# Performance work log

Measured on AMD Instinct MI355X. Metric: run time of the kernel, lower is better.

Reference implementation:

```python
import jax, jax.numpy as jnp
import numpy as np

B, S, D, H = 1, 4096, 1024, 16
HD = D // H  # head_size = 64

def setup_inputs() -> dict:
    key = jax.random.key(0)
    ks = jax.random.split(key, 9)
    scale = 1.0 / np.sqrt(D)
    return {
        "x": jax.random.normal(ks[0], (B, S, D), jnp.float32),
        "Wq": jax.random.normal(ks[1], (D, D), jnp.float32) * scale,
        "bq": jax.random.normal(ks[2], (D,), jnp.float32) * 0.01,
        "Wk": jax.random.normal(ks[3], (D, D), jnp.float32) * scale,
        "bk": jax.random.normal(ks[4], (D,), jnp.float32) * 0.01,
        "Wv": jax.random.normal(ks[5], (D, D), jnp.float32) * scale,
        "bv": jax.random.normal(ks[6], (D,), jnp.float32) * 0.01,
        "Wo": jax.random.normal(ks[7], (D, D), jnp.float32) * scale,
        "bo": jax.random.normal(ks[8], (D,), jnp.float32) * 0.01,
    }

def _split_heads(t):
    # (B, S, D) -> (B, H, S, HD)
    return t.reshape(B, S, H, HD).transpose(0, 2, 1, 3)

def reference(x, Wq, bq, Wk, bk, Wv, bv, Wo, bo):
    q = _split_heads(x @ Wq + bq)
    k = _split_heads(x @ Wk + bk)
    v = _split_heads(x @ Wv + bv)
    # scores: (B, H, S, S), materialized as in the original naive attention
    scores = jnp.einsum('bhqd,bhkd->bhqk', q, k) / jnp.sqrt(jnp.asarray(HD, q.dtype))
    causal = jnp.tril(jnp.ones((S, S), dtype=bool))  # tril mask, broadcast over (B, H)
    scores = jnp.where(causal[None, None], scores, jnp.asarray(-1e9, scores.dtype))
    attn = jax.nn.softmax(scores, axis=-1)
    out = jnp.einsum('bhqk,bhkd->bhqd', attn, v)  # (B, H, S, HD)
    out = out.transpose(0, 2, 1, 3).reshape(B, S, D)  # combine heads
    return out @ Wo + bo
```

## Files before the change

kernel.cpp:

```cpp
#include <hip/hip_runtime.h>

#define SEQ 4096
#define DM  1024
#define NH  16
#define HDIM 64

typedef unsigned short u16;
typedef unsigned int   u32;
typedef __bf16 bf16x8 __attribute__((ext_vector_type(8)));
typedef float f32x4 __attribute__((ext_vector_type(4)));

__device__ __forceinline__ float bf2f(u16 u) {
    unsigned v = ((unsigned)u) << 16;
    float f;
    __builtin_memcpy(&f, &v, 4);
    return f;
}
__device__ __forceinline__ u16 f2bf(float f) {
    unsigned u;
    __builtin_memcpy(&u, &f, 4);
    return (u16)((u + 0x7fffu + ((u >> 16) & 1u)) >> 16);
}
__device__ __forceinline__ u32 bfpack(float a, float b) {
    u32 ua, ub;
    __builtin_memcpy(&ua, &a, 4);
    __builtin_memcpy(&ub, &b, 4);
    return ((ua + 0x8000u) >> 16) | ((ub + 0x8000u) & 0xffff0000u);
}

typedef const __attribute__((address_space(1))) unsigned int gas_uint;
typedef __attribute__((address_space(3))) unsigned int las_uint;
__device__ __forceinline__ void gld16(const u16* g, u16* l) {
    __builtin_amdgcn_global_load_lds((gas_uint*)g, (las_uint*)l, 16, 0, 0);
}

__device__ __forceinline__ f32x4 mfma16(bf16x8 a, bf16x8 b, f32x4 c) {
    return __builtin_amdgcn_mfma_f32_16x16x32_bf16(a, b, c, 0, 0, 0);
}

#define QSCALE 0.18033688011f

__device__ __forceinline__ int self_detect(const void* in, int tid, int* sflag) {
    if (tid == 0) *sflag = 0;
    __syncthreads();
    const u16* p = (const u16*)in;
    int loc = 0;
    for (int i = tid; i < 4096; i += 256) {
        float v = fabsf(bf2f(p[i]));
        if (v < 3e38f && v > 1e4f) loc = 1;
    }
    if (loc) *sflag = 1;
    __syncthreads();
    return *sflag;
}

__global__ __launch_bounds__(256) void prep_all(const void* w0, const void* w1,
                                                const void* w2, const void* w3,
                                                const void* b0, const void* b1,
                                                const void* b2, const void* b3,
                                                const void* xin,
                                                u16* __restrict__ wt,
                                                u16* __restrict__ b_dst,
                                                u16* __restrict__ xc,
                                                int* __restrict__ flags) {
    __shared__ int sflag;
    __shared__ u16 tile[32][33];
    const int z   = blockIdx.z;
    const int tid = threadIdx.x;
    const void* srcs[5] = {w0, w1, w2, w3, xin};
    const void* in = srcs[z];
    const int f = self_detect(in, tid, &sflag);

    if (z == 4) {
        const int p = blockIdx.y * 32 + blockIdx.x;
        if (p == 0 && tid == 0) flags[0] = f;
#pragma unroll
        for (int c = 0; c < 2; ++c) {
            const size_t i = (size_t)p * 4096 + c * 2048 + tid * 8;
            if (f) {
                const float4* s4 = (const float4*)((const float*)in + i);
                float4 a = s4[0], bq = s4[1];
                uint4 o;
                o.x = bfpack(a.x, a.y);
                o.y = bfpack(a.z, a.w);
                o.z = bfpack(bq.x, bq.y);
                o.w = bfpack(bq.z, bq.w);
                *(uint4*)(xc + i) = o;
            } else {
                *(uint4*)(xc + i) = *(const uint4*)((const u16*)in + i);
            }
        }
        return;
    }

    const void* bins[4] = {b0, b1, b2, b3};
    u16* out = wt + (size_t)z * DM * DM;
    const float scale = (z == 0) ? QSCALE : 1.0f;
    const int bx = blockIdx.x * 32;
    const int by = blockIdx.y * 32;
    const int tx = tid & 31;
    const int ty = tid >> 5;
#pragma unroll
    for (int i = ty; i < 32; i += 8) {
        size_t idx = (size_t)(by + i) * DM + bx + tx;
        float v = f ? ((const float*)in)[idx] : bf2f(((const u16*)in)[idx]);
        tile[i][tx] = f2bf(v * scale);
    }
    __syncthreads();
#pragma unroll
    for (int i = ty; i < 32; i += 8) out[(size_t)(bx + i) * DM + by + tx] = tile[tx][i];

    if (blockIdx.x == 0 && blockIdx.y == 0) {
        const void* bi = bins[z];
        for (int i = tid; i < DM; i += 256) {
            float v = f ? ((const float*)bi)[i] : bf2f(((const u16*)bi)[i]);
            b_dst[z * DM + i] = f2bf(v * scale);
        }
    }
}

__global__ __launch_bounds__(256, 2) void gemm_qkv(const u16* __restrict__ A,
                                                   const u16* __restrict__ Bt,
                                                   const u16* __restrict__ bias,
                                                   u16* __restrict__ Qo,
                                                   u16* __restrict__ Ko,
                                                   u16* __restrict__ VtO) {
    __shared__ u16 As[128 * 32];
    __shared__ u16 Bs[128 * 32];
    const int tid  = threadIdx.x;
    const int lane = tid & 63;
    const int w    = tid >> 6;
    const int m    = lane & 15;
    const int quad = lane >> 4;
    const int wr   = w >> 1;
    const int wc   = w & 1;

    const int b   = blockIdx.x;
    const int x   = b & 7;
    const int j   = b >> 3;
    const int nb  = (x * 3 + j % 3) * 128;
    const int mb  = (j / 3) * 128;
    const int mat = nb >> 10;
    const int lnb = nb & 1023;

    f32x4 acc[4][4] = {};

    for (int kb = 0; kb < DM; kb += 32) {
        __syncthreads();
#pragma unroll
        for (int i = 0; i < 2; ++i) {
            const int Lb = i * 256 + w * 64;
            const int L  = Lb + lane;
            const int row = L >> 2, cb = L & 3;
            gld16(&A[(size_t)(mb + row) * DM + kb + cb * 8], &As[Lb * 8]);
            gld16(&Bt[(size_t)(nb + row) * DM + kb + cb * 8], &Bs[Lb * 8]);
        }
        __syncthreads();

        bf16x8 af[4];
#pragma unroll
        for (int mt = 0; mt < 4; ++mt)
            af[mt] = *(const bf16x8*)&As[(wr * 64 + mt * 16 + m) * 32 + quad * 8];
#pragma unroll
        for (int ct = 0; ct < 4; ++ct) {
            bf16x8 bfr = *(const bf16x8*)&Bs[(wc * 64 + ct * 16 + m) * 32 + quad * 8];
#pragma unroll
            for (int mt = 0; mt < 4; ++mt)
                acc[mt][ct] = mfma16(af[mt], bfr, acc[mt][ct]);
        }
    }

    if (mat < 2) {
        u16* C = mat ? Ko : Qo;
#pragma unroll
        for (int ct = 0; ct < 4; ++ct) {
            float bv = bf2f(bias[nb + wc * 64 + ct * 16 + m]);
#pragma unroll
            for (int mt = 0; mt < 4; ++mt)
#pragma unroll
                for (int r = 0; r < 4; ++r) {
                    int row = mb + wr * 64 + mt * 16 + quad * 4 + r;
                    C[(size_t)row * DM + lnb + wc * 64 + ct * 16 + m] =
                        f2bf(acc[mt][ct][r] + bv);
                }
        }
    } else {
#pragma unroll
        for (int ct = 0; ct < 4; ++ct) {
            const int n = lnb + wc * 64 + ct * 16 + m;
            float bv = bf2f(bias[nb + wc * 64 + ct * 16 + m]);
#pragma unroll
            for (int mt = 0; mt < 4; ++mt) {
                const int rowb = mb + wr * 64 + mt * 16 + quad * 4;
                uint2 pk;
                pk.x = bfpack(acc[mt][ct][0] + bv, acc[mt][ct][1] + bv);
                pk.y = bfpack(acc[mt][ct][2] + bv, acc[mt][ct][3] + bv);
                *(uint2*)&VtO[(size_t)n * SEQ + rowb] = pk;
            }
        }
    }
}

__global__ __launch_bounds__(256, 2) void gemm_n64(const u16* __restrict__ A,
                                                   const u16* __restrict__ Bt,
                                                   const u16* __restrict__ bias,
                                                   void* __restrict__ C,
                                                   const int* __restrict__ flags) {
    __shared__ u16 As[128 * 32];
    __shared__ u16 Bs[64 * 32];
    const int f    = flags[0];
    const int tid  = threadIdx.x;
    const int lane = tid & 63;
    const int w    = tid >> 6;
    const int m    = lane & 15;
    const int quad = lane >> 4;

    const int b  = blockIdx.x;
    const int x  = b & 7;
    const int j  = b >> 3;
    const int nb = (x * 2 + (j & 1)) * 64;
    const int mb = (j >> 1) * 128;

    f32x4 acc[2][4] = {};

    for (int kb = 0; kb < DM; kb += 32) {
        __syncthreads();
#pragma unroll
        for (int i = 0; i < 2; ++i) {
            const int Lb = (2 * w + i) * 64;
            const int L  = Lb + lane;
            const int row = L >> 2, cb = L & 3;
            gld16(&A[(size_t)(mb + row) * DM + kb + cb * 8], &As[Lb * 8]);
        }
        {
            const int L = w * 64 + lane;
            const int row = L >> 2, cb = L & 3;
            gld16(&Bt[(size_t)(nb + row) * DM + kb + cb * 8], &Bs[w * 512]);
        }
        __syncthreads();

        bf16x8 af[2];
#pragma unroll
        for (int mt = 0; mt < 2; ++mt)
            af[mt] = *(const bf16x8*)&As[(w * 32 + mt * 16 + m) * 32 + quad * 8];
#pragma unroll
        for (int ct = 0; ct < 4; ++ct) {
            bf16x8 bfr = *(const bf16x8*)&Bs[(ct * 16 + m) * 32 + quad * 8];
#pragma unroll
            for (int mt = 0; mt < 2; ++mt)
                acc[mt][ct] = mfma16(af[mt], bfr, acc[mt][ct]);
        }
    }

#pragma unroll
    for (int ct = 0; ct < 4; ++ct) {
        float bv = bf2f(bias[nb + ct * 16 + m]);
#pragma unroll
        for (int mt = 0; mt < 2; ++mt) {
#pragma unroll
            for (int r = 0; r < 4; ++r) {
                int row = mb + w * 32 + mt * 16 + quad * 4 + r;
                size_t idx = (size_t)row * DM + nb + ct * 16 + m;
                float v = acc[mt][ct][r] + bv;
                if (f) ((float*)C)[idx] = v;
                else   ((u16*)C)[idx]   = f2bf(v);
            }
        }
    }
}

__global__ __launch_bounds__(256, 2) void attn_split(const u16* __restrict__ Qb,
                                                     const u16* __restrict__ Kb,
                                                     const u16* __restrict__ Vt,
                                                     u16* __restrict__ slot0,
                                                     u16* __restrict__ slot1,
                                                     u16* __restrict__ slot2,
                                                     float* __restrict__ l0,
                                                     float* __restrict__ l1,
                                                     float* __restrict__ l2) {
    __shared__ u16 Ks[2][128 * 64];
    __shared__ u16 Vs[2][64 * 128];

    const int tid  = threadIdx.x;
    const int lane = tid & 63;
    const int w    = tid >> 6;
    const int m    = lane & 15;
    const int quad = lane >> 4;
    const int l3   = lane >> 3;
    const int l4   = lane >> 4;
    const int m7   = m & 7;
    const int cxk  = ((lane & 7) ^ l3) * 8;

    const int b    = blockIdx.x;
    const int x    = b & 7;
    const int u    = b >> 3;
    const int qt2  = 15 - (u / 6);
    const int v6   = u % 6;
    const int head = 2 * x + (v6 / 3);
    const int part = v6 % 3;
    const int hc   = head * HDIM;
    const int n128 = 2 * qt2 + 2;
    const int k0t  = part * n128 / 3;
    const int k1t  = (part + 1) * n128 / 3 - 1;

    const int qw = qt2 * 256 + w * 64;
    const int dw = qw >> 6;

    bf16x8 qf[4][2];
#pragma unroll
    for (int qt4 = 0; qt4 < 4; ++qt4)
#pragma unroll
        for (int c = 0; c < 2; ++c)
            qf[qt4][c] = *(const bf16x8*)&Qb[(size_t)(qw + qt4 * 16 + m) * DM + hc + c * 32 + quad * 8];

    f32x4 o_acc[4][4] = {};
    float l_part[4] = {0.f, 0.f, 0.f, 0.f};

#pragma unroll
    for (int i = 0; i < 4; ++i) {
        const int kr = w * 32 + i * 8 + l3;
        gld16(&Kb[(size_t)(k0t * 128 + kr) * DM + hc + cxk], &Ks[0][(w * 32 + i * 8) * 64]);
        const int vr = w * 16 + i * 4 + l4;
        const int cxv = ((lane & 15) ^ ((i * 4 + l4) & 7)) * 8;
        gld16(&Vt[(size_t)(hc + vr) * SEQ + k0t * 128 + cxv], &Vs[0][(w * 16 + i * 4) * 128]);
    }

    for (int kt = k0t; kt <= k1t; ++kt) {
        const int cur = (kt - k0t) & 1;
        __syncthreads();

        if (kt < k1t) {
            const int nbf = 1 - cur;
            const int nkt = kt + 1;
#pragma unroll
            for (int i = 0; i < 4; ++i) {
                const int kr = w * 32 + i * 8 + l3;
                gld16(&Kb[(size_t)(nkt * 128 + kr) * DM + hc + cxk], &Ks[nbf][(w * 32 + i * 8) * 64]);
                const int vr = w * 16 + i * 4 + l4;
                const int cxv = ((lane & 15) ^ ((i * 4 + l4) & 7)) * 8;
                gld16(&Vt[(size_t)(hc + vr) * SEQ + nkt * 128 + cxv], &Vs[nbf][(w * 16 + i * 4) * 128]);
            }
        }

        const u16* ksb = Ks[cur];
        const u16* vsb = Vs[cur];

#pragma unroll
        for (int h = 0; h < 2; ++h) {
            const int t64 = kt * 2 + h;
            if (t64 > dw) continue;

#pragma unroll
            for (int p = 0; p < 2; ++p) {
                const int ph = 2 * h + p;
                uint4 pa_raw[4];

#pragma unroll
                for (int stt = 0; stt < 2; ++stt) {
                    const int st = ph * 2 + stt;
                    bf16x8 kf[2];
#pragma unroll
                    for (int c = 0; c < 2; ++c)
                        kf[c] = *(const bf16x8*)&ksb[(st * 16 + m) * 64 + (((c * 4 + quad) ^ m7) * 8)];

                    f32x4 sc[4];
#pragma unroll
                    for (int qt4 = 0; qt4 < 4; ++qt4) {
                        f32x4 a = {};
                        a = mfma16(kf[0], qf[qt4][0], a);
                        a = mfma16(kf[1], qf[qt4][1], a);
                        sc[qt4] = a;
                    }

                    if (t64 == dw) {
                        const int stl = 2 * p + stt;
#pragma unroll
                        for (int qt4 = 0; qt4 < 4; ++qt4)
#pragma unroll
                            for (int r = 0; r < 4; ++r) {
                                float pp = __builtin_amdgcn_exp2f(sc[qt4][r]);
                                sc[qt4][r] = (stl * 16 + quad * 4 + r > qt4 * 16 + m) ? 0.f : pp;
                            }
                    } else {
#pragma unroll
                        for (int qt4 = 0; qt4 < 4; ++qt4)
#pragma unroll
                            for (int r = 0; r < 4; ++r)
                                sc[qt4][r] = __builtin_amdgcn_exp2f(sc[qt4][r]);
                    }

#pragma unroll
                    for (int qt4 = 0; qt4 < 4; ++qt4) {
                        l_part[qt4] += sc[qt4][0] + sc[qt4][1] + sc[qt4][2] + sc[qt4][3];
                        const u32 pk0 = bfpack(sc[qt4][0], sc[qt4][1]);
                        const u32 pk1 = bfpack(sc[qt4][2], sc[qt4][3]);
                        if (stt == 0) { pa_raw[qt4].x = pk0; pa_raw[qt4].y = pk1; }
                        else          { pa_raw[qt4].z = pk0; pa_raw[qt4].w = pk1; }
                    }
                }

                bf16x8 pa[4];
#pragma unroll
                for (int qt4 = 0; qt4 < 4; ++qt4) __builtin_memcpy(&pa[qt4], &pa_raw[qt4], 16);

#pragma unroll
                for (int dt = 0; dt < 4; ++dt) {
                    const int base = (dt * 16 + m) * 128;
                    const int clo = ((4 * ph + (quad >> 1)) ^ m7) * 8 + (quad & 1) * 4;
                    const int chi = ((4 * ph + 2 + (quad >> 1)) ^ m7) * 8 + (quad & 1) * 4;
                    uint2 vlo = *(const uint2*)&vsb[base + clo];
                    uint2 vhi = *(const uint2*)&vsb[base + chi];
                    uint4 t;
                    t.x = vlo.x; t.y = vlo.y; t.z = vhi.x; t.w = vhi.y;
                    bf16x8 vf;
                    __builtin_memcpy(&vf, &t, 16);
#pragma unroll
                    for (int qt4 = 0; qt4 < 4; ++qt4)
                        o_acc[qt4][dt] = mfma16(pa[qt4], vf, o_acc[qt4][dt]);
                }
            }
        }
    }

#pragma unroll
    for (int qt4 = 0; qt4 < 4; ++qt4) {
        l_part[qt4] += __shfl_xor(l_part[qt4], 16, 64);
        l_part[qt4] += __shfl_xor(l_part[qt4], 32, 64);
    }

    u16*   dst = (part == 0) ? slot0 : ((part == 1) ? slot1 : slot2);
    float* lb  = (part == 0) ? l0 : ((part == 1) ? l1 : l2);
#pragma unroll
    for (int qt4 = 0; qt4 < 4; ++qt4)
#pragma unroll
        for (int dt = 0; dt < 4; ++dt)
#pragma unroll
            for (int r = 0; r < 4; ++r) {
                int row = qw + qt4 * 16 + quad * 4 + r;
                dst[(size_t)row * DM + hc + dt * 16 + m] = f2bf(o_acc[qt4][dt][r]);
            }
    if (lane < 16) {
#pragma unroll
        for (int qt4 = 0; qt4 < 4; ++qt4)
            lb[head * SEQ + qw + qt4 * 16 + lane] = l_part[qt4];
    }
}

__global__ __launch_bounds__(256) void merge_k(u16* __restrict__ s0,
                                               const u16* __restrict__ s1,
                                               const u16* __restrict__ s2,
                                               const float* __restrict__ l0,
                                               const float* __restrict__ l1,
                                               const float* __restrict__ l2) {
    const int gid = blockIdx.x * 256 + threadIdx.x;
    const int rl = gid >> 7;
    const int cg = gid & 127;
    const int h  = cg >> 3;
    const float inv = 1.0f / (l0[h * SEQ + rl] + l1[h * SEQ + rl] + l2[h * SEQ + rl]);
    uint4 va = *(const uint4*)(s0 + (size_t)rl * DM + cg * 8);
    uint4 vb = *(const uint4*)(s1 + (size_t)rl * DM + cg * 8);
    uint4 vc = *(const uint4*)(s2 + (size_t)rl * DM + cg * 8);
    const u16* a16 = (const u16*)&va;
    const u16* b16 = (const u16*)&vb;
    const u16* c16 = (const u16*)&vc;
    u16 oo[8];
#pragma unroll
    for (int i = 0; i < 8; ++i)
        oo[i] = f2bf((bf2f(a16[i]) + bf2f(b16[i]) + bf2f(c16[i])) * inv);
    *(uint4*)(s0 + (size_t)rl * DM + cg * 8) = *(const uint4*)&oo[0];
}

extern "C" void kernel_launch(void* const* d_in, const int* in_sizes, int n_in,
                              void* d_out, int out_size, void* d_ws, size_t ws_size,
                              hipStream_t stream) {
    (void)in_sizes; (void)n_in; (void)out_size; (void)ws_size;

    u16* ws    = (u16*)d_ws;
    int* flags = (int*)d_ws;
    u16* xc    = ws + 64;
    u16* Wtqkv = xc + (size_t)SEQ * DM;
    u16* Wto   = Wtqkv + (size_t)3 * DM * DM;
    u16* bqkv  = Wto + (size_t)DM * DM;
    u16* boc   = bqkv + 3 * DM;
    u16* Qb    = boc + DM;
    u16* Kb    = Qb + (size_t)SEQ * DM;
    u16* Vt_g  = Kb + (size_t)SEQ * DM;
    u16* ab    = Vt_g + (size_t)SEQ * DM;
    u16* slotB = ab + (size_t)SEQ * DM;
    u16* slotC = xc;
    float* l0f = (float*)Wtqkv;
    float* l1f = l0f + NH * SEQ;
    float* l2f = l1f + NH * SEQ;

    prep_all<<<dim3(32, 32, 5), 256, 0, stream>>>(
        d_in[1], d_in[3], d_in[5], d_in[7],
        d_in[2], d_in[4], d_in[6], d_in[8],
        d_in[0], Wtqkv, bqkv, xc, flags);

    gemm_qkv<<<dim3(768), 256, 0, stream>>>(xc, Wtqkv, bqkv, Qb, Kb, Vt_g);

    attn_split<<<dim3(768), 256, 0, stream>>>(Qb, Kb, Vt_g, ab, slotB, slotC,
                                              l0f, l1f, l2f);

    merge_k<<<dim3(SEQ * 128 / 256), 256, 0, stream>>>(ab, slotB, slotC, l0f, l1f, l2f);

    gemm_n64<<<dim3(512), 256, 0, stream>>>(ab, Wto, boc, d_out, flags);
}
```

Baseline: 224.4 us.

## Use K=64 swizzled LDS tiles and split-K output GEMM with bias-add pass

```diff
diff --git a/kernel.cpp b/kernel.cpp
--- a/kernel.cpp
+++ b/kernel.cpp
@@ -125,8 +125,8 @@
                                                    u16* __restrict__ Qo,
                                                    u16* __restrict__ Ko,
                                                    u16* __restrict__ VtO) {
-    __shared__ u16 As[128 * 32];
-    __shared__ u16 Bs[128 * 32];
+    __shared__ u16 As[128 * 64];
+    __shared__ u16 Bs[128 * 64];
     const int tid  = threadIdx.x;
     const int lane = tid & 63;
     const int w    = tid >> 6;
@@ -134,6 +134,7 @@
     const int quad = lane >> 4;
     const int wr   = w >> 1;
     const int wc   = w & 1;
+    const int m7   = m & 7;
 
     const int b   = blockIdx.x;
     const int x   = b & 7;
@@ -145,28 +146,35 @@
 
     f32x4 acc[4][4] = {};
 
-    for (int kb = 0; kb < DM; kb += 32) {
+    for (int kb = 0; kb < DM; kb += 64) {
         __syncthreads();
 #pragma unroll
-        for (int i = 0; i < 2; ++i) {
-            const int Lb = i * 256 + w * 64;
+        for (int i = 0; i < 4; ++i) {
+            const int Lb = w * 256 + i * 64;
             const int L  = Lb + lane;
-            const int row = L >> 2, cb = L & 3;
-            gld16(&A[(size_t)(mb + row) * DM + kb + cb * 8], &As[Lb * 8]);
-            gld16(&Bt[(size_t)(nb + row) * DM + kb + cb * 8], &Bs[Lb * 8]);
+            const int row = L >> 3, cb = L & 7;
+            const int gc = (cb ^ (row & 7)) * 8;
+            gld16(&A[(size_t)(mb + row) * DM + kb + gc], &As[Lb * 8]);
+            gld16(&Bt[(size_t)(nb + row) * DM + kb + gc], &Bs[Lb * 8]);
         }
         __syncthreads();
 
-        bf16x8 af[4];
+        bf16x8 af[4][2];
 #pragma unroll
         for (int mt = 0; mt < 4; ++mt)
-            af[mt] = *(const bf16x8*)&As[(wr * 64 + mt * 16 + m) * 32 + quad * 8];
+#pragma unroll
+            for (int c = 0; c < 2; ++c)
+                af[mt][c] = *(const bf16x8*)&As[(wr * 64 + mt * 16 + m) * 64 + (((c * 4 + quad) ^ m7) * 8)];
 #pragma unroll
         for (int ct = 0; ct < 4; ++ct) {
-            bf16x8 bfr = *(const bf16x8*)&Bs[(wc * 64 + ct * 16 + m) * 32 + quad * 8];
-#pragma unroll
-            for (int mt = 0; mt < 4; ++mt)
-                acc[mt][ct] = mfma16(af[mt], bfr, acc[mt][ct]);
+            const int rb = (wc * 64 + ct * 16 + m) * 64;
+            bf16x8 b0 = *(const bf16x8*)&Bs[rb + (((0 + quad) ^ m7) * 8)];
+            bf16x8 b1 = *(const bf16x8*)&Bs[rb + (((4 + quad) ^ m7) * 8)];
+#pragma unroll
+            for (int mt = 0; mt < 4; ++mt) {
+                acc[mt][ct] = mfma16(af[mt][0], b0, acc[mt][ct]);
+                acc[mt][ct] = mfma16(af[mt][1], b1, acc[mt][ct]);
+            }
         }
     }
 
@@ -201,71 +209,102 @@
     }
 }
 
-__global__ __launch_bounds__(256, 2) void gemm_n64(const u16* __restrict__ A,
-                                                   const u16* __restrict__ Bt,
-                                                   const u16* __restrict__ bias,
-                                                   void* __restrict__ C,
-                                                   const int* __restrict__ flags) {
-    __shared__ u16 As[128 * 32];
-    __shared__ u16 Bs[64 * 32];
-    const int f    = flags[0];
+__global__ __launch_bounds__(256, 2) void gemm_osplit(const u16* __restrict__ A,
+                                                      const u16* __restrict__ Bt,
+                                                      u16* __restrict__ P0,
+                                                      u16* __restrict__ P1) {
+    __shared__ u16 As[128 * 64];
+    __shared__ u16 Bs[128 * 64];
     const int tid  = threadIdx.x;
     const int lane = tid & 63;
     const int w    = tid >> 6;
     const int m    = lane & 15;
     const int quad = lane >> 4;
+    const int wr   = w >> 1;
+    const int wc   = w & 1;
+    const int m7   = m & 7;
 
     const int b  = blockIdx.x;
     const int x  = b & 7;
     const int j  = b >> 3;
-    const int nb = (x * 2 + (j & 1)) * 64;
+    const int kp = j & 1;
     const int mb = (j >> 1) * 128;
-
-    f32x4 acc[2][4] = {};
-
-    for (int kb = 0; kb < DM; kb += 32) {
+    const int nb = x * 128;
+    const int kbase = kp * 512;
+
+    f32x4 acc[4][4] = {};
+
+    for (int kb = 0; kb < 512; kb += 64) {
         __syncthreads();
 #pragma unroll
-        for (int i = 0; i < 2; ++i) {
-            const int Lb = (2 * w + i) * 64;
+        for (int i = 0; i < 4; ++i) {
+            const int Lb = w * 256 + i * 64;
             const int L  = Lb + lane;
-            const int row = L >> 2, cb = L & 3;
-            gld16(&A[(size_t)(mb + row) * DM + kb + cb * 8], &As[Lb * 8]);
-        }
-        {
-            const int L = w * 64 + lane;
-            const int row = L >> 2, cb = L & 3;
-            gld16(&Bt[(size_t)(nb + row) * DM + kb + cb * 8], &Bs[w * 512]);
+            const int row = L >> 3, cb = L & 7;
+            const int gc = (cb ^ (row & 7)) * 8;
+            gld16(&A[(size_t)(mb + row) * DM + kbase + kb + gc], &As[Lb * 8]);
+            gld16(&Bt[(size_t)(nb + row) * DM + kbase + kb + gc], &Bs[Lb * 8]);
         }
         __syncthreads();
 
-        bf16x8 af[2];
-#pragma unroll
-        for (int mt = 0; mt < 2; ++mt)
-            af[mt] = *(const bf16x8*)&As[(w * 32 + mt * 16 + m) * 32 + quad * 8];
+        bf16x8 af[4][2];
+#pragma unroll
+        for (int mt = 0; mt < 4; ++mt)
+#pragma unroll
+            for (int c = 0; c < 2; ++c)
+                af[mt][c] = *(const bf16x8*)&As[(wr * 64 + mt * 16 + m) * 64 + (((c * 4 + quad) ^ m7) * 8)];
 #pragma unroll
         for (int ct = 0; ct < 4; ++ct) {
-            bf16x8 bfr = *(const bf16x8*)&Bs[(ct * 16 + m) * 32 + quad * 8];
-#pragma unroll
-            for (int mt = 0; mt < 2; ++mt)
-                acc[mt][ct] = mfma16(af[mt], bfr, acc[mt][ct]);
-        }
-    }
-
-#pragma unroll
-    for (int ct = 0; ct < 4; ++ct) {
-        float bv = bf2f(bias[nb + ct * 16 + m]);
-#pragma unroll
-        for (int mt = 0; mt < 2; ++mt) {
+            const int rb = (wc * 64 + ct * 16 + m) * 64;
+            bf16x8 b0 = *(const bf16x8*)&Bs[rb + (((0 + quad) ^ m7) * 8)];
+            bf16x8 b1 = *(const bf16x8*)&Bs[rb + (((4 + quad) ^ m7) * 8)];
+#pragma unroll
+            for (int mt = 0; mt < 4; ++mt) {
+                acc[mt][ct] = mfma16(af[mt][0], b0, acc[mt][ct]);
+                acc[mt][ct] = mfma16(af[mt][1], b1, acc[mt][ct]);
+            }
+        }
+    }
+
+    u16* P = kp ? P1 : P0;
+#pragma unroll
+    for (int ct = 0; ct < 4; ++ct)
+#pragma unroll
+        for (int mt = 0; mt < 4; ++mt)
 #pragma unroll
             for (int r = 0; r < 4; ++r) {
-                int row = mb + w * 32 + mt * 16 + quad * 4 + r;
-                size_t idx = (size_t)row * DM + nb + ct * 16 + m;
-                float v = acc[mt][ct][r] + bv;
-                if (f) ((float*)C)[idx] = v;
-                else   ((u16*)C)[idx]   = f2bf(v);
-            }
-        }
+                int row = mb + wr * 64 + mt * 16 + quad * 4 + r;
+                P[(size_t)row * DM + nb + wc * 64 + ct * 16 + m] = f2bf(acc[mt][ct][r]);
+            }
+}
+
+__global__ __launch_bounds__(256) void addb(const u16* __restrict__ P0,
+                                            const u16* __restrict__ P1,
+                                            const u16* __restrict__ bias,
+                                            void* __restrict__ out,
+                                            const int* __restrict__ flags) {
+    const int f = flags[0];
+    const size_t i = ((size_t)blockIdx.x * 256 + threadIdx.x) * 8;
+    const int n = (int)(i & 1023);
+    uint4 va = *(const uint4*)(P0 + i);
+    uint4 vb = *(const uint4*)(P1 + i);
+    const u16* a16 = (const u16*)&va;
+    const u16* b16 = (const u16*)&vb;
+    float v[8];
+#pragma unroll
+    for (int t = 0; t < 8; ++t)
+        v[t] = bf2f(a16[t]) + bf2f(b16[t]) + bf2f(bias[n + t]);
+    if (f) {
+        float4* o4 = (float4*)((float*)out + i);
+        o4[0] = make_float4(v[0], v[1], v[2], v[3]);
+        o4[1] = make_float4(v[4], v[5], v[6], v[7]);
+    } else {
+        uint4 o;
+        o.x = bfpack(v[0], v[1]);
+        o.y = bfpack(v[2], v[3]);
+        o.z = bfpack(v[4], v[5]);
+        o.w = bfpack(v[6], v[7]);
+        *(uint4*)((u16*)out + i) = o;
     }
 }
 
@@ -504,5 +543,6 @@
 
     merge_k<<<dim3(SEQ * 128 / 256), 256, 0, stream>>>(ab, slotB, slotC, l0f, l1f, l2f);
 
-    gemm_n64<<<dim3(512), 256, 0, stream>>>(ab, Wto, boc, d_out, flags);
-}
+    gemm_osplit<<<dim3(512), 256, 0, stream>>>(ab, Wto, slotC, slotB);
+    addb<<<dim3(SEQ * DM / 2048), 256, 0, stream>>>(slotC, slotB, boc, d_out, flags);
+}
```

New measurement: 217.2 us. -3.2%, faster.

## Deepen GEMM K-tile to 64 with XOR-swizzled LDS and compute row sums via MFMA

Applied to the files above, without the earlier changes.

```diff
diff --git a/kernel.cpp b/kernel.cpp
--- a/kernel.cpp
+++ b/kernel.cpp
@@ -125,8 +125,8 @@
                                                    u16* __restrict__ Qo,
                                                    u16* __restrict__ Ko,
                                                    u16* __restrict__ VtO) {
-    __shared__ u16 As[128 * 32];
-    __shared__ u16 Bs[128 * 32];
+    __shared__ u16 As[128 * 64];
+    __shared__ u16 Bs[128 * 64];
     const int tid  = threadIdx.x;
     const int lane = tid & 63;
     const int w    = tid >> 6;
@@ -134,6 +134,7 @@
     const int quad = lane >> 4;
     const int wr   = w >> 1;
     const int wc   = w & 1;
+    const int m7   = m & 7;
 
     const int b   = blockIdx.x;
     const int x   = b & 7;
@@ -145,28 +146,35 @@
 
     f32x4 acc[4][4] = {};
 
-    for (int kb = 0; kb < DM; kb += 32) {
+    for (int kb = 0; kb < DM; kb += 64) {
         __syncthreads();
 #pragma unroll
-        for (int i = 0; i < 2; ++i) {
-            const int Lb = i * 256 + w * 64;
+        for (int i = 0; i < 4; ++i) {
+            const int Lb = w * 256 + i * 64;
             const int L  = Lb + lane;
-            const int row = L >> 2, cb = L & 3;
-            gld16(&A[(size_t)(mb + row) * DM + kb + cb * 8], &As[Lb * 8]);
-            gld16(&Bt[(size_t)(nb + row) * DM + kb + cb * 8], &Bs[Lb * 8]);
+            const int row = L >> 3, cb = L & 7;
+            const int gc = (cb ^ (row & 7)) * 8;
+            gld16(&A[(size_t)(mb + row) * DM + kb + gc], &As[Lb * 8]);
+            gld16(&Bt[(size_t)(nb + row) * DM + kb + gc], &Bs[Lb * 8]);
         }
         __syncthreads();
 
-        bf16x8 af[4];
+        bf16x8 af[4][2];
 #pragma unroll
         for (int mt = 0; mt < 4; ++mt)
-            af[mt] = *(const bf16x8*)&As[(wr * 64 + mt * 16 + m) * 32 + quad * 8];
+#pragma unroll
+            for (int c = 0; c < 2; ++c)
+                af[mt][c] = *(const bf16x8*)&As[(wr * 64 + mt * 16 + m) * 64 + (((c * 4 + quad) ^ m7) * 8)];
 #pragma unroll
         for (int ct = 0; ct < 4; ++ct) {
-            bf16x8 bfr = *(const bf16x8*)&Bs[(wc * 64 + ct * 16 + m) * 32 + quad * 8];
-#pragma unroll
-            for (int mt = 0; mt < 4; ++mt)
-                acc[mt][ct] = mfma16(af[mt], bfr, acc[mt][ct]);
+            const int rb = (wc * 64 + ct * 16 + m) * 64;
+            bf16x8 b0 = *(const bf16x8*)&Bs[rb + (((0 + quad) ^ m7) * 8)];
+            bf16x8 b1 = *(const bf16x8*)&Bs[rb + (((4 + quad) ^ m7) * 8)];
+#pragma unroll
+            for (int mt = 0; mt < 4; ++mt) {
+                acc[mt][ct] = mfma16(af[mt][0], b0, acc[mt][ct]);
+                acc[mt][ct] = mfma16(af[mt][1], b1, acc[mt][ct]);
+            }
         }
     }
 
@@ -201,19 +209,20 @@
     }
 }
 
-__global__ __launch_bounds__(256, 2) void gemm_n64(const u16* __restrict__ A,
-                                                   const u16* __restrict__ Bt,
-                                                   const u16* __restrict__ bias,
-                                                   void* __restrict__ C,
-                                                   const int* __restrict__ flags) {
-    __shared__ u16 As[128 * 32];
-    __shared__ u16 Bs[64 * 32];
+__global__ __launch_bounds__(256, 2) void gemm_o(const u16* __restrict__ A,
+                                                 const u16* __restrict__ Bt,
+                                                 const u16* __restrict__ bias,
+                                                 void* __restrict__ C,
+                                                 const int* __restrict__ flags) {
+    __shared__ u16 As[128 * 64];
+    __shared__ u16 Bs[64 * 64];
     const int f    = flags[0];
     const int tid  = threadIdx.x;
     const int lane = tid & 63;
     const int w    = tid >> 6;
     const int m    = lane & 15;
     const int quad = lane >> 4;
+    const int m7   = m & 7;
 
     const int b  = blockIdx.x;
     const int x  = b & 7;
@@ -223,32 +232,42 @@
 
     f32x4 acc[2][4] = {};
 
-    for (int kb = 0; kb < DM; kb += 32) {
+    for (int kb = 0; kb < DM; kb += 64) {
         __syncthreads();
 #pragma unroll
+        for (int i = 0; i < 4; ++i) {
+            const int Lb = w * 256 + i * 64;
+            const int L  = Lb + lane;
+            const int row = L >> 3, cb = L & 7;
+            const int gc = (cb ^ (row & 7)) * 8;
+            gld16(&A[(size_t)(mb + row) * DM + kb + gc], &As[Lb * 8]);
+        }
+#pragma unroll
         for (int i = 0; i < 2; ++i) {
-            const int Lb = (2 * w + i) * 64;
+            const int Lb = w * 128 + i * 64;
             const int L  = Lb + lane;
-            const int row = L >> 2, cb = L & 3;
-            gld16(&A[(size_t)(mb + row) * DM + kb + cb * 8], &As[Lb * 8]);
-        }
-        {
-            const int L = w * 64 + lane;
-            const int row = L >> 2, cb = L & 3;
-            gld16(&Bt[(size_t)(nb + row) * DM + kb + cb * 8], &Bs[w * 512]);
+            const int row = L >> 3, cb = L & 7;
+            const int gc = (cb ^ (row & 7)) * 8;
+            gld16(&Bt[(size_t)(nb + row) * DM + kb + gc], &Bs[Lb * 8]);
         }
         __syncthreads();
 
-        bf16x8 af[2];
+        bf16x8 af[2][2];
 #pragma unroll
         for (int mt = 0; mt < 2; ++mt)
-            af[mt] = *(const bf16x8*)&As[(w * 32 + mt * 16 + m) * 32 + quad * 8];
+#pragma unroll
+            for (int c = 0; c < 2; ++c)
+                af[mt][c] = *(const bf16x8*)&As[(w * 32 + mt * 16 + m) * 64 + (((c * 4 + quad) ^ m7) * 8)];
 #pragma unroll
         for (int ct = 0; ct < 4; ++ct) {
-            bf16x8 bfr = *(const bf16x8*)&Bs[(ct * 16 + m) * 32 + quad * 8];
-#pragma unroll
-            for (int mt = 0; mt < 2; ++mt)
-                acc[mt][ct] = mfma16(af[mt], bfr, acc[mt][ct]);
+            const int rb = (ct * 16 + m) * 64;
+            bf16x8 b0 = *(const bf16x8*)&Bs[rb + (((0 + quad) ^ m7) * 8)];
+            bf16x8 b1 = *(const bf16x8*)&Bs[rb + (((4 + quad) ^ m7) * 8)];
+#pragma unroll
+            for (int mt = 0; mt < 2; ++mt) {
+                acc[mt][ct] = mfma16(af[mt][0], b0, acc[mt][ct]);
+                acc[mt][ct] = mfma16(af[mt][1], b1, acc[mt][ct]);
+            }
         }
     }
 
@@ -306,6 +325,13 @@
     const int qw = qt2 * 256 + w * 64;
     const int dw = qw >> 6;
 
+    bf16x8 onesf;
+    {
+        uint4 t1;
+        t1.x = t1.y = t1.z = t1.w = 0x3F803F80u;
+        __builtin_memcpy(&onesf, &t1, 16);
+    }
+
     bf16x8 qf[4][2];
 #pragma unroll
     for (int qt4 = 0; qt4 < 4; ++qt4)
@@ -314,7 +340,7 @@
             qf[qt4][c] = *(const bf16x8*)&Qb[(size_t)(qw + qt4 * 16 + m) * DM + hc + c * 32 + quad * 8];
 
     f32x4 o_acc[4][4] = {};
-    float l_part[4] = {0.f, 0.f, 0.f, 0.f};
+    f32x4 acc_l[4] = {};
 
 #pragma unroll
     for (int i = 0; i < 4; ++i) {
@@ -391,7 +417,6 @@
 
 #pragma unroll
                     for (int qt4 = 0; qt4 < 4; ++qt4) {
-                        l_part[qt4] += sc[qt4][0] + sc[qt4][1] + sc[qt4][2] + sc[qt4][3];
                         const u32 pk0 = bfpack(sc[qt4][0], sc[qt4][1]);
                         const u32 pk1 = bfpack(sc[qt4][2], sc[qt4][3]);
                         if (stt == 0) { pa_raw[qt4].x = pk0; pa_raw[qt4].y = pk1; }
@@ -402,6 +427,10 @@
                 bf16x8 pa[4];
 #pragma unroll
                 for (int qt4 = 0; qt4 < 4; ++qt4) __builtin_memcpy(&pa[qt4], &pa_raw[qt4], 16);
+
+#pragma unroll
+                for (int qt4 = 0; qt4 < 4; ++qt4)
+                    acc_l[qt4] = mfma16(pa[qt4], onesf, acc_l[qt4]);
 
 #pragma unroll
                 for (int dt = 0; dt < 4; ++dt) {
@@ -422,12 +451,6 @@
         }
     }
 
-#pragma unroll
-    for (int qt4 = 0; qt4 < 4; ++qt4) {
-        l_part[qt4] += __shfl_xor(l_part[qt4], 16, 64);
-        l_part[qt4] += __shfl_xor(l_part[qt4], 32, 64);
-    }
-
     u16*   dst = (part == 0) ? slot0 : ((part == 1) ? slot1 : slot2);
     float* lb  = (part == 0) ? l0 : ((part == 1) ? l1 : l2);
 #pragma unroll
@@ -439,10 +462,12 @@
                 int row = qw + qt4 * 16 + quad * 4 + r;
                 dst[(size_t)row * DM + hc + dt * 16 + m] = f2bf(o_acc[qt4][dt][r]);
             }
-    if (lane < 16) {
+    if (m == 0) {
 #pragma unroll
         for (int qt4 = 0; qt4 < 4; ++qt4)
-            lb[head * SEQ + qw + qt4 * 16 + lane] = l_part[qt4];
+#pragma unroll
+            for (int r = 0; r < 4; ++r)
+                lb[head * SEQ + qw + qt4 * 16 + quad * 4 + r] = acc_l[qt4][r];
     }
 }
 
@@ -504,5 +529,5 @@
 
     merge_k<<<dim3(SEQ * 128 / 256), 256, 0, stream>>>(ab, slotB, slotC, l0f, l1f, l2f);
 
-    gemm_n64<<<dim3(512), 256, 0, stream>>>(ab, Wto, boc, d_out, flags);
-}
+    gemm_o<<<dim3(512), 256, 0, stream>>>(ab, Wto, boc, d_out, flags);
+}
```

Measured after the change: 218.8 us. -2.5%, faster.
